# Performance work log

Hardware: AMD Instinct MI355X
Metric: run time of the kernel (lower is better)

Reference implementation:

```python
import jax, jax.numpy as jnp
import numpy as np

NEG_SLOPE = 0.2


def _build_dense_adj(edge_list, n):
    # edge_list: [2, E] int; symmetric 0/1 dense adjacency like edge_list_to_dense
    a = jnp.zeros((n, n), jnp.float32)
    a = a.at[edge_list[0], edge_list[1]].set(1.0)
    a = a.at[edge_list[1], edge_list[0]].set(1.0)
    return a


def setup_inputs() -> dict:
    key = jax.random.key(0)
    k1, k2, k3, k4 = jax.random.split(key, 4)
    N, T, D, H, E = 4096, 3, 16, 4, 65536
    scores = jax.random.normal(k1, (N, 1), jnp.float32)
    edge_type_emb = jax.random.normal(k2, (T, D), jnp.float32)
    att_w = jax.random.normal(k3, (H, D + 2, 1), jnp.float32) * 0.1  # xavier-ish
    edge_list = jax.random.randint(k4, (T, 2, E), 0, N, jnp.int64)
    return {"scores": scores, "edge_type_emb": edge_type_emb,
            "att_w": att_w, "edge_list": edge_list}


def reference(scores, edge_type_emb, att_w, edge_list):
    # scores: [N,1]; edge_type_emb: [T,D]; att_w: [H,D+2,1]; edge_list: [T,2,E]
    N = scores.shape[0]
    adjs = jax.vmap(lambda el: _build_dense_adj(el, N))(edge_list)  # [T,N,N]
    sum_adj = adjs.sum(axis=0)  # [N,N]
    s = scores[:, 0]            # [N]

    def head(w):
        w = w[:, 0]
        w_src, w_mid, w_tgt = w[0], w[1:-1], w[-1]
        # per-edge-type scalar from edge embedding dotted with middle weights
        c = edge_type_emb @ w_mid                    # [T]
        edge_term = jnp.einsum('tij,t->ij', adjs, c)  # [N,N]
        # (i,j): adj*(w_src*s_i) + adj*edge_emb.w_mid + adj*(w_tgt*s_j)
        logits = sum_adj * (w_src * s[:, None] + w_tgt * s[None, :]) + edge_term
        logits = jnp.where(logits >= 0, logits, NEG_SLOPE * logits)  # LeakyReLU
        att = jax.nn.softmax(logits, axis=-1)  # dense row softmax (as original)
        return att @ scores  # [N,1]

    outs = jax.vmap(head)(att_w)  # [H,N,1]
    return outs.mean(axis=0)      # average over heads
```

## Files before the change

kernel.cpp:

```cpp
#include <hip/hip_runtime.h>

#define NEG_SLOPE_F 0.2f

static constexpr int Nn = 4096;
static constexpr int Tt = 3;
static constexpr int Dd = 16;
static constexpr int Hh = 4;
static constexpr int CAP = 256;
static constexpr int BCAP = 96;

__device__ __forceinline__ float waveMax(float v) {
#pragma unroll
  for (int m = 1; m < 64; m <<= 1) v = fmaxf(v, __shfl_xor(v, m));
  return v;
}
__device__ __forceinline__ float waveSum(float v) {
#pragma unroll
  for (int m = 1; m < 64; m <<= 1) v += __shfl_xor(v, m);
  return v;
}

__global__ void clear_prep_kernel(unsigned int* __restrict__ cnt,
                                  const float* __restrict__ scores,
                                  const float* __restrict__ emb,
                                  const float* __restrict__ attw,
                                  float* __restrict__ pv) {
  int tid = threadIdx.x;
  int g = blockIdx.x * 256 + tid;
  if (g < Nn * Tt) cnt[g] = 0u;
  if (blockIdx.x == 0) {
    __shared__ float rb[4];
    float s = 0.f;
    for (int j = tid; j < Nn; j += 256) s += scores[j];
    s = waveSum(s);
    if ((tid & 63) == 0) rb[tid >> 6] = s;
    __syncthreads();
    if (tid == 0) pv[12] = rb[0] + rb[1] + rb[2] + rb[3];
    if (tid < Hh * Tt) {
      int h = tid / Tt, t = tid % Tt;
      float c = 0.f;
#pragma unroll
      for (int d = 0; d < Dd; ++d)
        c += emb[t * Dd + d] * attw[h * (Dd + 2) + 1 + d];
      pv[tid] = c;
    }
  }
}

__global__ void scatter_kernel(const int* __restrict__ el,
                               unsigned int* __restrict__ cnt,
                               unsigned short* __restrict__ slots, int E) {
  int k = blockIdx.x * blockDim.x + threadIdx.x;
  if (k >= Tt * E) return;
  int t = k / E, e = k - t * E;
  unsigned int a = (unsigned int)el[(t * 2 + 0) * E + e];
  unsigned int b = (unsigned int)el[(t * 2 + 1) * E + e];
  unsigned int pa = atomicAdd(&cnt[a * Tt + t], 1u);
  if (pa < BCAP) slots[(a * Tt + t) * BCAP + pa] = (unsigned short)b;
  unsigned int pb = atomicAdd(&cnt[b * Tt + t], 1u);
  if (pb < BCAP) slots[(b * Tt + t) * BCAP + pb] = (unsigned short)a;
}

__launch_bounds__(256)
__global__ void row_kernel(const unsigned int* __restrict__ cnt,
                           const unsigned short* __restrict__ slots,
                           const float* __restrict__ scores,
                           const float* __restrict__ attw,
                           const float* __restrict__ pv,
                           float* __restrict__ out) {
  __shared__ unsigned int bmL[4][Tt * 128];
  __shared__ unsigned short lst[4][CAP];
  int wid = threadIdx.x >> 6, lane = threadIdx.x & 63;
  int i = blockIdx.x * 4 + wid;
  unsigned int* bm = bmL[wid];

  for (int q = lane; q < Tt * 128; q += 64) bm[q] = 0u;

  int cv[Tt];
#pragma unroll
  for (int t = 0; t < Tt; ++t) {
    int c = (int)cnt[i * Tt + t];
    cv[t] = c < BCAP ? c : BCAP;
  }
  const unsigned short* sl = slots + (size_t)i * Tt * BCAP;
  for (int k = lane; k < Tt * BCAP; k += 64) {
    int t = k / BCAP, s = k - t * BCAP;
    if (s < cv[t]) {
      unsigned int j = (unsigned int)sl[k];
      atomicOr(&bm[t * 128 + (j >> 5)], 1u << (j & 31u));
    }
  }
  __syncthreads();

  unsigned int w[2][3];
#pragma unroll
  for (int p = 0; p < 2; ++p)
#pragma unroll
    for (int t = 0; t < 3; ++t) w[p][t] = bm[t * 128 + p * 64 + lane];
  unsigned int orw[2];
  orw[0] = w[0][0] | w[0][1] | w[0][2];
  orw[1] = w[1][0] | w[1][1] | w[1][2];
  int c = __popc(orw[0]) + __popc(orw[1]);
  int off = c;
#pragma unroll
  for (int d = 1; d < 64; d <<= 1) {
    int tv = __shfl_up(off, d);
    if (lane >= d) off += tv;
  }
  int n = __shfl(off, 63);
  off -= c;
  if (n > CAP) n = CAP;
  int idx = off;
#pragma unroll
  for (int p = 0; p < 2; ++p) {
    unsigned int o = orw[p];
    int jbase = (p * 64 + lane) * 32;
    while (o) {
      int b = __ffs(o) - 1;
      o &= o - 1;
      unsigned int m = ((w[p][0] >> b) & 1u) | (((w[p][1] >> b) & 1u) << 1) |
                       (((w[p][2] >> b) & 1u) << 2);
      if (idx < CAP) lst[wid][idx] = (unsigned short)((jbase + b) | (m << 12));
      ++idx;
    }
  }
  __syncthreads();

  float si = scores[i];
  float wsrc[Hh], wtgt[Hh], c0[Hh], c1[Hh], c2[Hh];
#pragma unroll
  for (int h = 0; h < Hh; ++h) {
    wsrc[h] = attw[h * (Dd + 2) + 0];
    wtgt[h] = attw[h * (Dd + 2) + Dd + 1];
    c0[h] = pv[h * 3 + 0];
    c1[h] = pv[h * 3 + 1];
    c2[h] = pv[h * 3 + 2];
  }
  float Ssum = pv[12];

  constexpr int IT = CAP / 64;
  float lv[IT][Hh], sjv[IT];
  float mx[Hh];
#pragma unroll
  for (int h = 0; h < Hh; ++h) mx[h] = -INFINITY;
  float sedge = 0.f;

#pragma unroll
  for (int it = 0; it < IT; ++it) {
    if (it * 64 >= n) break;
    int k = it * 64 + lane;
    bool act = k < n;
    unsigned int v = act ? (unsigned int)lst[wid][k] : 0u;
    int j = (int)(v & 0xFFFu);
    int m = act ? (int)(v >> 12) : 0;
    float sj = act ? scores[j] : 0.f;
    sjv[it] = sj;
    if (act) sedge += sj;
    float na = (float)__popc(m);
    float et0 = (m & 1) ? 1.f : 0.f;
    float et1 = (m & 2) ? 1.f : 0.f;
    float et2 = (m & 4) ? 1.f : 0.f;
#pragma unroll
    for (int h = 0; h < Hh; ++h) {
      float et = et0 * c0[h] + et1 * c1[h] + et2 * c2[h];
      float l = na * (wsrc[h] * si + wtgt[h] * sj) + et;
      l = (l >= 0.f) ? l : NEG_SLOPE_F * l;
      lv[it][h] = act ? l : -INFINITY;
      mx[h] = fmaxf(mx[h], lv[it][h]);
    }
  }

#pragma unroll
  for (int h = 0; h < Hh; ++h) {
    mx[h] = waveMax(mx[h]);
    if (n < Nn) mx[h] = fmaxf(mx[h], 0.f);
  }

  float se[Hh], ss[Hh];
#pragma unroll
  for (int h = 0; h < Hh; ++h) { se[h] = 0.f; ss[h] = 0.f; }
#pragma unroll
  for (int it = 0; it < IT; ++it) {
    if (it * 64 >= n) break;
#pragma unroll
    for (int h = 0; h < Hh; ++h) {
      float ex = expf(lv[it][h] - mx[h]);
      se[h] += ex;
      ss[h] += ex * sjv[it];
    }
  }
  sedge = waveSum(sedge);
#pragma unroll
  for (int h = 0; h < Hh; ++h) {
    se[h] = waveSum(se[h]);
    ss[h] = waveSum(ss[h]);
  }
  if (lane == 0) {
    float acc = 0.f;
#pragma unroll
    for (int h = 0; h < Hh; ++h) {
      float nz = expf(-mx[h]);
      float denom = se[h] + nz * ((float)Nn - (float)n);
      float numer = ss[h] + nz * (Ssum - sedge);
      acc += numer / denom;
    }
    out[i] = acc * (1.f / (float)Hh);
  }
}

extern "C" void kernel_launch(void* const* d_in, const int* in_sizes, int n_in,
                              void* d_out, int out_size, void* d_ws, size_t ws_size,
                              hipStream_t stream) {
  const float* scores = (const float*)d_in[0];
  const float* emb    = (const float*)d_in[1];
  const float* attw   = (const float*)d_in[2];
  const int*   el     = (const int*)d_in[3];
  float* out = (float*)d_out;
  int E = in_sizes[3] / (Tt * 2);

  unsigned int* cnt = (unsigned int*)d_ws;
  float* pv = (float*)((char*)d_ws + (size_t)Nn * Tt * 4);
  unsigned short* slots = (unsigned short*)((char*)pv + 64);

  clear_prep_kernel<<<(Nn * Tt + 255) / 256, 256, 0, stream>>>(cnt, scores, emb,
                                                               attw, pv);
  scatter_kernel<<<(Tt * (E) + 255) / 256, 256, 0, stream>>>(el, cnt, slots, E);
  row_kernel<<<Nn / 4, 256, 0, stream>>>(cnt, slots, scores, attw, pv, out);
}
```

Before: 41.65 us.

## Replace global-atomic edge scatter with block-local counting sort into per-row segments

```diff
diff --git a/kernel.cpp b/kernel.cpp
--- a/kernel.cpp
+++ b/kernel.cpp
@@ -7,7 +7,7 @@
 static constexpr int Dd = 16;
 static constexpr int Hh = 4;
 static constexpr int CAP = 256;
-static constexpr int BCAP = 96;
+static constexpr int NB = 128;
 
 __device__ __forceinline__ float waveMax(float v) {
 #pragma unroll
@@ -20,16 +20,38 @@
   return v;
 }
 
-__global__ void clear_prep_kernel(unsigned int* __restrict__ cnt,
-                                  const float* __restrict__ scores,
-                                  const float* __restrict__ emb,
-                                  const float* __restrict__ attw,
-                                  float* __restrict__ pv) {
-  int tid = threadIdx.x;
-  int g = blockIdx.x * 256 + tid;
-  if (g < Nn * Tt) cnt[g] = 0u;
+__global__ void hist_kernel(const int* __restrict__ el,
+                            unsigned int* __restrict__ ghist, int E) {
+  __shared__ unsigned int lh[Nn];
+  int tid = threadIdx.x, b = blockIdx.x;
+  for (int r = tid; r < Nn; r += 256) lh[r] = 0u;
+  __syncthreads();
+  int nE = Tt * E;
+  int per = (nE + NB - 1) / NB;
+  int k0 = b * per, k1 = k0 + per;
+  if (k1 > nE) k1 = nE;
+  for (int k = k0 + tid; k < k1; k += 256) {
+    int t = k / E, e = k - t * E;
+    unsigned int a = (unsigned int)el[(t * 2 + 0) * E + e];
+    unsigned int c = (unsigned int)el[(t * 2 + 1) * E + e];
+    atomicAdd(&lh[a], 1u);
+    atomicAdd(&lh[c], 1u);
+  }
+  __syncthreads();
+  unsigned int* gh = ghist + (size_t)b * Nn;
+  for (int r = tid; r < Nn; r += 256) gh[r] = lh[r];
+}
+
+__global__ void scan_prep_kernel(const unsigned int* __restrict__ ghist,
+                                 unsigned int* __restrict__ ofs,
+                                 unsigned int* __restrict__ cnt,
+                                 const float* __restrict__ scores,
+                                 const float* __restrict__ emb,
+                                 const float* __restrict__ attw,
+                                 float* __restrict__ pv) {
   if (blockIdx.x == 0) {
     __shared__ float rb[4];
+    int tid = threadIdx.x;
     float s = 0.f;
     for (int j = tid; j < Nn; j += 256) s += scores[j];
     s = waveSum(s);
@@ -45,25 +67,52 @@
       pv[tid] = c;
     }
   }
+  int wid = threadIdx.x >> 6, lane = threadIdx.x & 63;
+  int r = blockIdx.x * 4 + wid;
+  unsigned int a = ghist[(size_t)(2 * lane) * Nn + r];
+  unsigned int c = ghist[(size_t)(2 * lane + 1) * Nn + r];
+  unsigned int s = a + c;
+  unsigned int inc = s;
+#pragma unroll
+  for (int d = 1; d < 64; d <<= 1) {
+    unsigned int tv = __shfl_up(inc, d);
+    if (lane >= d) inc += tv;
+  }
+  unsigned int excl = inc - s;
+  unsigned int base = (unsigned int)r * CAP;
+  ofs[(size_t)(2 * lane) * Nn + r] = base + excl;
+  ofs[(size_t)(2 * lane + 1) * Nn + r] = base + excl + a;
+  if (lane == 63) cnt[r] = inc;
 }
 
 __global__ void scatter_kernel(const int* __restrict__ el,
-                               unsigned int* __restrict__ cnt,
-                               unsigned short* __restrict__ slots, int E) {
-  int k = blockIdx.x * blockDim.x + threadIdx.x;
-  if (k >= Tt * E) return;
-  int t = k / E, e = k - t * E;
-  unsigned int a = (unsigned int)el[(t * 2 + 0) * E + e];
-  unsigned int b = (unsigned int)el[(t * 2 + 1) * E + e];
-  unsigned int pa = atomicAdd(&cnt[a * Tt + t], 1u);
-  if (pa < BCAP) slots[(a * Tt + t) * BCAP + pa] = (unsigned short)b;
-  unsigned int pb = atomicAdd(&cnt[b * Tt + t], 1u);
-  if (pb < BCAP) slots[(b * Tt + t) * BCAP + pb] = (unsigned short)a;
+                               const unsigned int* __restrict__ ofs,
+                               unsigned short* __restrict__ seg, int E) {
+  __shared__ unsigned int lofs[Nn];
+  int tid = threadIdx.x, b = blockIdx.x;
+  const unsigned int* ob = ofs + (size_t)b * Nn;
+  for (int r = tid; r < Nn; r += 256) lofs[r] = ob[r];
+  __syncthreads();
+  int nE = Tt * E;
+  int per = (nE + NB - 1) / NB;
+  int k0 = b * per, k1 = k0 + per;
+  if (k1 > nE) k1 = nE;
+  for (int k = k0 + tid; k < k1; k += 256) {
+    int t = k / E, e = k - t * E;
+    unsigned int a = (unsigned int)el[(t * 2 + 0) * E + e];
+    unsigned int c = (unsigned int)el[(t * 2 + 1) * E + e];
+    unsigned int pa = atomicAdd(&lofs[a], 1u);
+    if (pa - a * (unsigned)CAP < (unsigned)CAP)
+      seg[pa] = (unsigned short)(c | ((unsigned)t << 12));
+    unsigned int pc = atomicAdd(&lofs[c], 1u);
+    if (pc - c * (unsigned)CAP < (unsigned)CAP)
+      seg[pc] = (unsigned short)(a | ((unsigned)t << 12));
+  }
 }
 
 __launch_bounds__(256)
-__global__ void row_kernel(const unsigned int* __restrict__ cnt,
-                           const unsigned short* __restrict__ slots,
+__global__ void row_kernel(const unsigned short* __restrict__ seg,
+                           const unsigned int* __restrict__ cnt,
                            const float* __restrict__ scores,
                            const float* __restrict__ attw,
                            const float* __restrict__ pv,
@@ -75,22 +124,14 @@
   unsigned int* bm = bmL[wid];
 
   for (int q = lane; q < Tt * 128; q += 64) bm[q] = 0u;
-
-  int cv[Tt];
-#pragma unroll
-  for (int t = 0; t < Tt; ++t) {
-    int c = (int)cnt[i * Tt + t];
-    cv[t] = c < BCAP ? c : BCAP;
-  }
-  const unsigned short* sl = slots + (size_t)i * Tt * BCAP;
-  for (int k = lane; k < Tt * BCAP; k += 64) {
-    int t = k / BCAP, s = k - t * BCAP;
-    if (s < cv[t]) {
-      unsigned int j = (unsigned int)sl[k];
-      atomicOr(&bm[t * 128 + (j >> 5)], 1u << (j & 31u));
-    }
-  }
-  __syncthreads();
+  int nd = (int)cnt[i];
+  if (nd > CAP) nd = CAP;
+  const unsigned short* sg = seg + (size_t)i * CAP;
+  for (int k = lane; k < nd; k += 64) {
+    unsigned int v = (unsigned int)sg[k];
+    unsigned int col = v & 0xFFFu, t = v >> 12;
+    atomicOr(&bm[t * 128 + (col >> 5)], 1u << (col & 31u));
+  }
 
   unsigned int w[2][3];
 #pragma unroll
@@ -124,7 +165,6 @@
       ++idx;
     }
   }
-  __syncthreads();
 
   float si = scores[i];
   float wsrc[Hh], wtgt[Hh], c0[Hh], c1[Hh], c2[Hh];
@@ -218,12 +258,15 @@
   float* out = (float*)d_out;
   int E = in_sizes[3] / (Tt * 2);
 
-  unsigned int* cnt = (unsigned int*)d_ws;
-  float* pv = (float*)((char*)d_ws + (size_t)Nn * Tt * 4);
-  unsigned short* slots = (unsigned short*)((char*)pv + 64);
-
-  clear_prep_kernel<<<(Nn * Tt + 255) / 256, 256, 0, stream>>>(cnt, scores, emb,
-                                                               attw, pv);
-  scatter_kernel<<<(Tt * (E) + 255) / 256, 256, 0, stream>>>(el, cnt, slots, E);
-  row_kernel<<<Nn / 4, 256, 0, stream>>>(cnt, slots, scores, attw, pv, out);
-}
+  unsigned int* ghist = (unsigned int*)d_ws;
+  unsigned int* ofs = ghist + (size_t)NB * Nn;
+  unsigned int* cnt = ofs + (size_t)NB * Nn;
+  float* pv = (float*)(cnt + Nn);
+  unsigned short* seg = (unsigned short*)((char*)pv + 64);
+
+  hist_kernel<<<NB, 256, 0, stream>>>(el, ghist, E);
+  scan_prep_kernel<<<Nn / 4, 256, 0, stream>>>(ghist, ofs, cnt, scores, emb,
+                                               attw, pv);
+  scatter_kernel<<<NB, 256, 0, stream>>>(el, ofs, seg, E);
+  row_kernel<<<Nn / 4, 256, 0, stream>>>(seg, cnt, scores, attw, pv, out);
+}
```

After: 37.27 us. 1.12x faster.
